# Kernel optimization log

Hardware: AMD Instinct MI355X
Metric: run time of the kernel (lower is better)

## Reference

```python
import jax, jax.numpy as jnp
import numpy as np

N, F_IN, C, H, L = 4096, 768, 256, 4, 2
DH = C // H  # 64 per-head dim for GATv2


def _ln(x, g, b, eps=1e-5):
    mu = x.mean(-1, keepdims=True)
    var = ((x - mu) ** 2).mean(-1, keepdims=True)
    return (x - mu) / jnp.sqrt(var + eps) * g + b


def _gat_layer(x, wl, wr, att, b, src, dst):
    # GATv2Conv: e_ij = att . leaky_relu(Wl x_j + Wr x_i); softmax over incoming j; concat heads.
    xs = (x @ wl).reshape(N, H, DH)  # source transform
    xd = (x @ wr).reshape(N, H, DH)  # target transform
    e = jnp.einsum('ehd,hd->eh', jax.nn.leaky_relu(xs[src] + xd[dst], 0.2), att)  # [E,H]
    m = jax.ops.segment_max(e, dst, num_segments=N)          # segment softmax (stable)
    p = jnp.exp(e - m[dst])
    s = jax.ops.segment_sum(p, dst, num_segments=N)
    alpha = p / (s[dst] + 1e-16)                             # [E,H]
    out = jax.ops.segment_sum(alpha[:, :, None] * xs[src], dst, num_segments=N)
    return out.reshape(N, C) + b


def _mha(x, wq, wk, wv, bq, bk, bv, wo, bo):
    # nn.MultiheadAttention, batch=1 sequence of all news nodes, eval mode.
    q = (x @ wq + bq).reshape(N, H, DH)
    k = (x @ wk + bk).reshape(N, H, DH)
    v = (x @ wv + bv).reshape(N, H, DH)
    scale = np.float32(1.0 / np.sqrt(DH))
    a = jax.nn.softmax(jnp.einsum('nhd,mhd->hnm', q, k) * scale, axis=-1)  # [H,N,N]
    o = jnp.einsum('hnm,mhd->nhd', a, v).reshape(N, C)
    return o @ wo + bo


def setup_inputs() -> dict:
    key = jax.random.key(0)
    ks = jax.random.split(key, 32)
    rn = lambda k, shp: (jax.random.normal(k, shp, dtype=jnp.float32) * 0.02)
    inp = {
        'x': jax.random.normal(ks[0], (N, F_IN), dtype=jnp.float32),
        'edge_index': jax.random.randint(ks[1], (2, N * 64), 0, N, dtype=jnp.int64),
        'emb_w': rn(ks[2], (F_IN, C)), 'emb_b': jnp.zeros((C,), jnp.float32),
        'g1_wl': rn(ks[3], (C, C)), 'g1_wr': rn(ks[4], (C, C)),
        'g1_att': rn(ks[5], (H, DH)), 'g1_b': jnp.zeros((C,), jnp.float32),
        'g2_wl': rn(ks[6], (C, C)), 'g2_wr': rn(ks[7], (C, C)),
        'g2_att': rn(ks[8], (H, DH)), 'g2_b': jnp.zeros((C,), jnp.float32),
        'mha_wq': rn(ks[9], (C, C)), 'mha_wk': rn(ks[10], (C, C)), 'mha_wv': rn(ks[11], (C, C)),
        'mha_bq': jnp.zeros((C,), jnp.float32), 'mha_bk': jnp.zeros((C,), jnp.float32),
        'mha_bv': jnp.zeros((C,), jnp.float32),
        'mha_wo': rn(ks[12], (C, C)), 'mha_bo': jnp.zeros((C,), jnp.float32),
        'ln_g': jnp.ones((C,), jnp.float32), 'ln_b': jnp.zeros((C,), jnp.float32),
        'cls_w1': rn(ks[13], (C, C // 2)), 'cls_b1': jnp.zeros((C // 2,), jnp.float32),
        'cls_w2': rn(ks[14], (C // 2, 2)), 'cls_b2': jnp.zeros((2,), jnp.float32),
    }
    return inp


def reference(x, edge_index, emb_w, emb_b, g1_wl, g1_wr, g1_att, g1_b,
              g2_wl, g2_wr, g2_att, g2_b, mha_wq, mha_wk, mha_wv, mha_bq,
              mha_bk, mha_bv, mha_wo, mha_bo, ln_g, ln_b,
              cls_w1, cls_b1, cls_w2, cls_b2):
    # add self loops (GATv2Conv default add_self_loops=True)
    loops = jnp.arange(N, dtype=edge_index.dtype)
    src = jnp.concatenate([edge_index[0], loops])
    dst = jnp.concatenate([edge_index[1], loops])

    h = x @ emb_w + emb_b                              # node embedding Linear(-1, C)
    h = jax.nn.relu(_gat_layer(h, g1_wl, g1_wr, g1_att, g1_b, src, dst))
    h = jax.nn.relu(_gat_layer(h, g2_wl, g2_wr, g2_att, g2_b, src, dst))

    # entity-aware self-attention + residual LayerNorm
    enh = _mha(h, mha_wq, mha_wk, mha_wv, mha_bq, mha_bk, mha_bv, mha_wo, mha_bo)
    h = _ln(h + enh, ln_g, ln_b)

    # classifier MLP (dropout = identity in eval)
    h = jax.nn.relu(h @ cls_w1 + cls_b1)
    return h @ cls_w2 + cls_b2
```

## Files before the change

kernel.cpp:

```cpp
#include <hip/hip_runtime.h>

typedef __attribute__((ext_vector_type(8))) short short8_t;
typedef __attribute__((ext_vector_type(4))) float f32x4_t;

#define N_NODES  4096
#define E0_EDGES 262144
#define E_TOTAL  266240
#define SPLITS   8
#define KV_PER_SPLIT (N_NODES / SPLITS)

__device__ __forceinline__ float bf2f(unsigned short u){
  union { unsigned int i; float f; } v; v.i = ((unsigned int)u) << 16; return v.f;
}
__device__ __forceinline__ unsigned short f2bf(float f){
  union { float f; unsigned int i; } v; v.f = f;
  unsigned int r = (v.i + 0x7FFFu + ((v.i >> 16) & 1u)) >> 16;
  return (unsigned short)r;
}
__device__ __forceinline__ unsigned int cvtpk_bf16(float lo, float hi){
  unsigned int r;
  asm volatile("v_cvt_pk_bf16_f32 %0, %1, %2" : "=v"(r) : "v"(lo), "v"(hi));
  return r;
}
template<int CTRL>
__device__ __forceinline__ float dpp_add(float x){
  int v = __builtin_amdgcn_update_dpp(0, __float_as_int(x), CTRL, 0xF, 0xF, true);
  return x + __int_as_float(v);
}
__device__ __forceinline__ float rowsum16(float x){
  x = dpp_add<0xB1>(x); x = dpp_add<0x4E>(x); x = dpp_add<0x124>(x); x = dpp_add<0x128>(x);
  return x;
}
__device__ __forceinline__ void wg_barrier(){
  asm volatile("s_waitcnt lgkmcnt(0)" ::: "memory");
  __builtin_amdgcn_s_barrier();
  asm volatile("" ::: "memory");
}
__device__ __forceinline__ uint4 cvt8_f32_to_bf16(float4 f0, float4 f1){
  union { unsigned short u[8]; uint4 q; } o;
  o.u[0]=f2bf(f0.x); o.u[1]=f2bf(f0.y); o.u[2]=f2bf(f0.z); o.u[3]=f2bf(f0.w);
  o.u[4]=f2bf(f1.x); o.u[5]=f2bf(f1.y); o.u[6]=f2bf(f1.z); o.u[7]=f2bf(f1.w);
  return o.q;
}

struct TJob { const float* src; unsigned short* dst; int rows, cols, tile0; };
struct TJobs { TJob j[10]; };

__global__ __launch_bounds__(256) void prep_kernel(TJobs jobs, int tb, int* __restrict__ zp){
  __shared__ unsigned short tile[64 * 64];
  int b = blockIdx.x, t = threadIdx.x;
  if (b < tb){
    int ji = 0;
    #pragma unroll
    for (int k = 1; k < 10; k++) if (b >= jobs.j[k].tile0) ji = k;
    TJob J = jobs.j[ji];
    int lt = b - J.tile0;
    int tpr = J.cols >> 6;
    int tr = lt / tpr, tc = lt - tr * tpr;
    #pragma unroll
    for (int i2 = 0; i2 < 2; i2++){
      int e = i2 * 2048 + t * 8;
      int nl = e >> 6, c8 = e & 63;
      const float* sp = &J.src[(size_t)(tr * 64 + nl) * J.cols + tc * 64 + c8];
      float4 v0 = *(const float4*)sp;
      float4 v1 = *(const float4*)(sp + 4);
      *(uint4*)&tile[nl * 64 + (((c8 >> 3) ^ ((nl >> 3) & 7)) * 8)] = cvt8_f32_to_bf16(v0, v1);
    }
    __syncthreads();
    #pragma unroll
    for (int i2 = 0; i2 < 2; i2++){
      int e = i2 * 2048 + t * 8;
      int cl = e >> 6, n8 = e & 63;
      union { unsigned short u[8]; uint4 q; } o;
      #pragma unroll
      for (int j = 0; j < 8; j++){
        int row = n8 + j;
        o.u[j] = tile[row * 64 + (((cl >> 3) ^ ((row >> 3) & 7)) * 8) + (cl & 7)];
      }
      *(uint4*)&J.dst[(size_t)(tc * 64 + cl) * J.rows + tr * 64 + n8] = o.q;
    }
    return;
  }
  int i = (b - tb) * 256 + t;
  if (i < 8192) zp[i] = 0;
}

__global__ __launch_bounds__(256) void scatter_kernel(const int* __restrict__ ei, const int* __restrict__ offs,
                                                      int* __restrict__ cur, int* __restrict__ csrc){
  int e = blockIdx.x * 256 + threadIdx.x;
  if (e >= E_TOTAL) return;
  int s, d;
  if (e < E0_EDGES){ s = ei[e]; d = ei[E0_EDGES + e]; }
  else { s = d = e - E0_EDGES; }
  int pos = offs[d] + atomicAdd(&cur[d], 1);
  csrc[pos] = s;
}

struct GJob { const unsigned short* Wt; const float* bias; float* outF; unsigned short* outB; unsigned short* outT; float scale; };
struct GJobs { GJob j[3]; };
struct AuxJob { int mode; const int* ei; int* a; int* b; };

__global__ __launch_bounds__(256) void gemm_kernel(const unsigned short* __restrict__ A, const float* __restrict__ Af32,
                                                   GJobs jobs, int K, int Nc, int relu, AuxJob AX){
  __shared__ unsigned short lds[8192];
  const int t = threadIdx.x;

  if (AX.mode && blockIdx.z == gridDim.z - 1){
    int flat = blockIdx.x + (blockIdx.y << 6);
    if (AX.mode == 1){
      for (int e = flat * 256 + t; e < E_TOTAL; e += 65536){
        int d = (e < E0_EDGES) ? AX.ei[E0_EDGES + e] : (e - E0_EDGES);
        atomicAdd(&AX.a[d], 1);
      }
    } else if (flat == 0){
      int* wtot = (int*)lds;
      int lane = t & 63, w = t >> 6;
      int v[16];
      int base = t * 16;
      int s = 0;
      #pragma unroll
      for (int j = 0; j < 16; j++){ v[j] = AX.a[base + j]; s += v[j]; }
      int x = s;
      #pragma unroll
      for (int off = 1; off < 64; off <<= 1){
        int y = __shfl_up(x, off, 64);
        if (lane >= off) x += y;
      }
      if (lane == 63) wtot[w] = x;
      __syncthreads();
      int wbase = 0;
      #pragma unroll
      for (int k = 0; k < 4; k++) if (k < w) wbase += wtot[k];
      int run = wbase + x - s;
      #pragma unroll
      for (int j = 0; j < 16; j++){ AX.b[base + j] = run; run += v[j]; }
      if (t == 255) AX.b[N_NODES] = run;
    }
    return;
  }

  const GJob job = jobs.j[blockIdx.z];
  const int lane = t & 63, w = t >> 6;
  const int wm = w >> 1, wn = w & 1;
  const int c16 = lane & 15, g = lane >> 4;
  const int bm = blockIdx.x, bn = blockIdx.y;

  const int srow = t >> 2, schunk = t & 3;
  const unsigned short* Ag = Af32 ? nullptr : (A + (size_t)(bm * 64 + srow) * K + schunk * 8);
  const float* Ag32 = Af32 ? (Af32 + (size_t)(bm * 64 + srow) * K + schunk * 8) : nullptr;
  const unsigned short* Bg = job.Wt + (size_t)(bn * 64 + srow) * K + schunk * 8;
  const int swz = srow * 32 + ((schunk ^ ((srow >> 1) & 3)) * 8);

  const int arow0 = wm * 32 + c16, arow1 = arow0 + 16;
  const int aoff0 = arow0 * 32 + ((g ^ ((arow0 >> 1) & 3)) * 8);
  const int aoff1 = arow1 * 32 + ((g ^ ((arow1 >> 1) & 3)) * 8);
  const int bcol0 = wn * 32 + c16, bcol1 = bcol0 + 16;
  const int boff0 = 2048 + bcol0 * 32 + ((g ^ ((bcol0 >> 1) & 3)) * 8);
  const int boff1 = 2048 + bcol1 * 32 + ((g ^ ((bcol1 >> 1) & 3)) * 8);

  f32x4_t acc[2][2] = {};
  const int nk = K >> 5;

  {
    uint4 av;
    if (Af32){
      float4 f0 = *(const float4*)(Ag32);
      float4 f1 = *(const float4*)(Ag32 + 4);
      av = cvt8_f32_to_bf16(f0, f1);
    } else {
      av = *(const uint4*)(Ag);
    }
    uint4 bv = *(const uint4*)(Bg);
    *(uint4*)&lds[swz]        = av;
    *(uint4*)&lds[2048 + swz] = bv;
  }
  int cur = 0;
  for (int i = 0; i < nk; i++){
    const bool pf = (i + 1) < nk;
    uint4 av, bv;
    float4 af0, af1;
    if (pf){
      if (Af32){
        af0 = *(const float4*)(Ag32 + (i + 1) * 32);
        af1 = *(const float4*)(Ag32 + (i + 1) * 32 + 4);
      } else {
        av = *(const uint4*)(Ag + (i + 1) * 32);
      }
      bv = *(const uint4*)(Bg + (i + 1) * 32);
    }
    wg_barrier();
    const int base = cur * 4096;
    union { uint4 u; short8_t s; } a0, a1, b0, b1;
    a0.u = *(const uint4*)&lds[base + aoff0];
    a1.u = *(const uint4*)&lds[base + aoff1];
    b0.u = *(const uint4*)&lds[base + boff0];
    b1.u = *(const uint4*)&lds[base + boff1];
    acc[0][0] = __builtin_amdgcn_mfma_f32_16x16x32_bf16(a0.s, b0.s, acc[0][0], 0, 0, 0);
    acc[0][1] = __builtin_amdgcn_mfma_f32_16x16x32_bf16(a0.s, b1.s, acc[0][1], 0, 0, 0);
    acc[1][0] = __builtin_amdgcn_mfma_f32_16x16x32_bf16(a1.s, b0.s, acc[1][0], 0, 0, 0);
    acc[1][1] = __builtin_amdgcn_mfma_f32_16x16x32_bf16(a1.s, b1.s, acc[1][1], 0, 0, 0);
    if (pf){
      const int nb = (cur ^ 1) * 4096;
      if (Af32) av = cvt8_f32_to_bf16(af0, af1);
      *(uint4*)&lds[nb + swz]        = av;
      *(uint4*)&lds[nb + 2048 + swz] = bv;
      cur ^= 1;
    }
  }

  #pragma unroll
  for (int fm = 0; fm < 2; fm++){
    #pragma unroll
    for (int fn = 0; fn < 2; fn++){
      int col = bn * 64 + wn * 32 + fn * 16 + c16;
      float bia = job.bias ? job.bias[col] : 0.f;
      float vv[4];
      #pragma unroll
      for (int r = 0; r < 4; r++){
        float v = (acc[fm][fn][r] + bia) * job.scale;
        if (relu) v = fmaxf(v, 0.f);
        vv[r] = v;
      }
      int row0 = bm * 64 + wm * 32 + fm * 16 + g * 4;
      if (job.outF){
        #pragma unroll
        for (int r = 0; r < 4; r++) job.outF[(size_t)(row0 + r) * Nc + col] = vv[r];
      }
      if (job.outB){
        #pragma unroll
        for (int r = 0; r < 4; r++) job.outB[(size_t)(row0 + r) * Nc + col] = f2bf(vv[r]);
      }
      if (job.outT){
        union { unsigned short u[4]; uint2 q; } pk;
        #pragma unroll
        for (int r = 0; r < 4; r++) pk.u[r] = f2bf(vv[r]);
        *(uint2*)&job.outT[(size_t)col * 4096 + row0] = pk.q;
      }
    }
  }
}

__global__ __launch_bounds__(256) void gat_gather(const unsigned short* __restrict__ xs, const unsigned short* __restrict__ xd,
                                                  const float* __restrict__ att, const float* __restrict__ bias,
                                                  const int* __restrict__ offs, const int* __restrict__ csrc,
                                                  unsigned short* __restrict__ outB, float* __restrict__ outF){
  __shared__ float combL[4][256];
  __shared__ float combS[4][4];
  const int i = blockIdx.x, t = threadIdx.x;
  const int lane = t & 63, w = t >> 6;
  float xdc[4], attc[4];
  {
    uint2 xv = *(const uint2*)&xd[i * 256 + lane * 4];
    xdc[0] = bf2f((unsigned short)(xv.x & 0xffff)); xdc[1] = bf2f((unsigned short)(xv.x >> 16));
    xdc[2] = bf2f((unsigned short)(xv.y & 0xffff)); xdc[3] = bf2f((unsigned short)(xv.y >> 16));
    float4 av = *(const float4*)&att[lane * 4];
    attc[0] = av.x; attc[1] = av.y; attc[2] = av.z; attc[3] = av.w;
  }
  const int b0 = offs[i], b1 = offs[i + 1];
  float acc0 = 0.f, acc1 = 0.f, acc2 = 0.f, acc3 = 0.f, ssum = 0.f;
  int p = b0 + w;
  for (; p + 4 < b1; p += 8){
    int sA = csrc[p], sB = csrc[p + 4];
    uint2 xa = *(const uint2*)&xs[sA * 256 + lane * 4];
    uint2 xb = *(const uint2*)&xs[sB * 256 + lane * 4];
    float a0 = bf2f((unsigned short)(xa.x & 0xffff)), a1 = bf2f((unsigned short)(xa.x >> 16));
    float a2 = bf2f((unsigned short)(xa.y & 0xffff)), a3 = bf2f((unsigned short)(xa.y >> 16));
    float b0_ = bf2f((unsigned short)(xb.x & 0xffff)), b1_ = bf2f((unsigned short)(xb.x >> 16));
    float b2_ = bf2f((unsigned short)(xb.y & 0xffff)), b3_ = bf2f((unsigned short)(xb.y >> 16));
    float va0 = a0 + xdc[0]; va0 = (va0 > 0.f) ? va0 : 0.2f * va0;
    float va1 = a1 + xdc[1]; va1 = (va1 > 0.f) ? va1 : 0.2f * va1;
    float va2 = a2 + xdc[2]; va2 = (va2 > 0.f) ? va2 : 0.2f * va2;
    float va3 = a3 + xdc[3]; va3 = (va3 > 0.f) ? va3 : 0.2f * va3;
    float vb0 = b0_ + xdc[0]; vb0 = (vb0 > 0.f) ? vb0 : 0.2f * vb0;
    float vb1 = b1_ + xdc[1]; vb1 = (vb1 > 0.f) ? vb1 : 0.2f * vb1;
    float vb2 = b2_ + xdc[2]; vb2 = (vb2 > 0.f) ? vb2 : 0.2f * vb2;
    float vb3 = b3_ + xdc[3]; vb3 = (vb3 > 0.f) ? vb3 : 0.2f * vb3;
    float eA = rowsum16(va0 * attc[0] + va1 * attc[1] + va2 * attc[2] + va3 * attc[3]);
    float eB = rowsum16(vb0 * attc[0] + vb1 * attc[1] + vb2 * attc[2] + vb3 * attc[3]);
    float pA = __expf(eA), pB = __expf(eB);
    ssum += pA + pB;
    acc0 += pA * a0 + pB * b0_; acc1 += pA * a1 + pB * b1_;
    acc2 += pA * a2 + pB * b2_; acc3 += pA * a3 + pB * b3_;
  }
  if (p < b1){
    int s = csrc[p];
    uint2 xv = *(const uint2*)&xs[s * 256 + lane * 4];
    float x0 = bf2f((unsigned short)(xv.x & 0xffff)), x1 = bf2f((unsigned short)(xv.x >> 16));
    float x2 = bf2f((unsigned short)(xv.y & 0xffff)), x3 = bf2f((unsigned short)(xv.y >> 16));
    float v0 = x0 + xdc[0]; v0 = (v0 > 0.f) ? v0 : 0.2f * v0;
    float v1 = x1 + xdc[1]; v1 = (v1 > 0.f) ? v1 : 0.2f * v1;
    float v2 = x2 + xdc[2]; v2 = (v2 > 0.f) ? v2 : 0.2f * v2;
    float v3 = x3 + xdc[3]; v3 = (v3 > 0.f) ? v3 : 0.2f * v3;
    float e = rowsum16(v0 * attc[0] + v1 * attc[1] + v2 * attc[2] + v3 * attc[3]);
    float pe = __expf(e);
    ssum += pe;
    acc0 += pe * x0; acc1 += pe * x1; acc2 += pe * x2; acc3 += pe * x3;
  }
  combL[w][lane * 4 + 0] = acc0; combL[w][lane * 4 + 1] = acc1;
  combL[w][lane * 4 + 2] = acc2; combL[w][lane * 4 + 3] = acc3;
  if ((lane & 15) == 0) combS[w][lane >> 4] = ssum;
  __syncthreads();
  float atot = combL[0][t] + combL[1][t] + combL[2][t] + combL[3][t];
  int hh = t >> 6;
  float stot = combS[0][hh] + combS[1][hh] + combS[2][hh] + combS[3][hh];
  float o = atot / (stot + 1e-16f) + bias[t];
  o = fmaxf(o, 0.f);
  outB[i * 256 + t] = f2bf(o);
  if (outF) outF[i * 256 + t] = o;
}

__global__ __launch_bounds__(512, 2) void attn_kernel(const unsigned short* __restrict__ qb, const unsigned short* __restrict__ kb,
                                                      const unsigned short* __restrict__ vt,
                                                      _Float16* __restrict__ Opart, float* __restrict__ Ol){
  __shared__ unsigned short K_lds[2][4096];
  __shared__ unsigned short V_lds[2][4096];
  __shared__ unsigned short P_lds[8][2048];
  const int t = threadIdx.x, lane = t & 63, w = t >> 6;
  const int c16 = lane & 15, g = lane >> 4;
  const int h = blockIdx.y, bq = blockIdx.x, sp = blockIdx.z;

  const int sr = t >> 3, sc = (t & 7) * 8;
  const int kw = sr * 64 + (((t & 7) ^ ((sr >> 1) & 7)) * 8);
  const int vw = sr * 64 + (((t & 7) ^ (sr & 7)) * 8);

  short8_t qa[2][2];
  #pragma unroll
  for (int qm = 0; qm < 2; qm++){
    int qrow = bq * 256 + w * 32 + qm * 16 + c16;
    union { uint4 u; short8_t s; } cv0, cv1;
    cv0.u = *(const uint4*)&qb[(size_t)qrow * 256 + h * 64 + g * 8];
    cv1.u = *(const uint4*)&qb[(size_t)qrow * 256 + h * 64 + 32 + g * 8];
    qa[qm][0] = cv0.s; qa[qm][1] = cv1.s;
  }

  f32x4_t oacc[2][4] = {};
  float lsum[2] = {0.f, 0.f};

  const int kv_lo = sp * KV_PER_SPLIT;
  {
    uint4 k0 = *(const uint4*)&kb[(size_t)(kv_lo + sr) * 256 + h * 64 + sc];
    uint4 v0 = *(const uint4*)&vt[(size_t)(h * 64 + sr) * 4096 + kv_lo + sc];
    *(uint4*)&K_lds[0][kw] = k0;
    *(uint4*)&V_lds[0][vw] = v0;
  }
  int cur = 0;

  for (int ti = 0; ti < KV_PER_SPLIT / 64; ti++){
    const bool pf = (ti + 1) < KV_PER_SPLIT / 64;
    uint4 nk, nv;
    if (pf){
      int kvn = kv_lo + (ti + 1) * 64;
      nk = *(const uint4*)&kb[(size_t)(kvn + sr) * 256 + h * 64 + sc];
      nv = *(const uint4*)&vt[(size_t)(h * 64 + sr) * 4096 + kvn + sc];
    }
    wg_barrier();
    const unsigned short* Kb = K_lds[cur];
    const unsigned short* Vb = V_lds[cur];
    unsigned short* Pw = P_lds[w];

    f32x4_t sacc[2][4] = {};
    #pragma unroll
    for (int kd = 0; kd < 2; kd++){
      #pragma unroll
      for (int fn = 0; fn < 4; fn++){
        union { uint4 u; short8_t s; } kf;
        kf.u = *(const uint4*)&Kb[(fn * 16 + c16) * 64 + (((kd * 4 + g) ^ ((c16 >> 1) & 7)) * 8)];
        sacc[0][fn] = __builtin_amdgcn_mfma_f32_16x16x32_bf16(kf.s, qa[0][kd], sacc[0][fn], 0, 0, 0);
        sacc[1][fn] = __builtin_amdgcn_mfma_f32_16x16x32_bf16(kf.s, qa[1][kd], sacc[1][fn], 0, 0, 0);
      }
    }

    #pragma unroll
    for (int qm = 0; qm < 2; qm++){
      float ps = 0.f;
      int row = qm * 16 + c16;
      #pragma unroll
      for (int fn = 0; fn < 4; fn++){
        float p0 = __builtin_exp2f(sacc[qm][fn][0]);
        float p1 = __builtin_exp2f(sacc[qm][fn][1]);
        float p2 = __builtin_exp2f(sacc[qm][fn][2]);
        float p3 = __builtin_exp2f(sacc[qm][fn][3]);
        ps += (p0 + p1) + (p2 + p3);
        uint2 pk;
        pk.x = cvtpk_bf16(p0, p1);
        pk.y = cvtpk_bf16(p2, p3);
        int chunk = (fn * 2 + (g >> 1)) ^ (c16 & 7);
        *(uint2*)&Pw[row * 64 + chunk * 8 + (g & 1) * 4] = pk;
      }
      ps += __shfl_xor(ps, 16, 64);
      ps += __shfl_xor(ps, 32, 64);
      lsum[qm] += ps;
    }

    #pragma unroll
    for (int kd2 = 0; kd2 < 2; kd2++){
      const int ch = (((kd2 * 4 + g) ^ (c16 & 7)) * 8);
      union { uint4 u; short8_t s; } pt0, pt1;
      pt0.u = *(const uint4*)&Pw[c16 * 64 + ch];
      pt1.u = *(const uint4*)&Pw[(16 + c16) * 64 + ch];
      #pragma unroll
      for (int fn = 0; fn < 4; fn++){
        union { uint4 u; short8_t s; } vf;
        vf.u = *(const uint4*)&Vb[(fn * 16 + c16) * 64 + ch];
        oacc[0][fn] = __builtin_amdgcn_mfma_f32_16x16x32_bf16(vf.s, pt0.s, oacc[0][fn], 0, 0, 0);
        oacc[1][fn] = __builtin_amdgcn_mfma_f32_16x16x32_bf16(vf.s, pt1.s, oacc[1][fn], 0, 0, 0);
      }
    }

    if (pf){
      *(uint4*)&K_lds[cur ^ 1][kw] = nk;
      *(uint4*)&V_lds[cur ^ 1][vw] = nv;
      cur ^= 1;
    }
  }

  const int sh = sp * 4 + h;
  #pragma unroll
  for (int qm = 0; qm < 2; qm++){
    int node = bq * 256 + w * 32 + qm * 16 + c16;
    #pragma unroll
    for (int fn = 0; fn < 4; fn++){
      union { _Float16 h[4]; uint2 q; } pk;
      #pragma unroll
      for (int r = 0; r < 4; r++) pk.h[r] = (_Float16)oacc[qm][fn][r];
      *(uint2*)&Opart[((size_t)sh * N_NODES + node) * 64 + fn * 16 + g * 4] = pk.q;
    }
    if (g == 0) Ol[(size_t)sh * N_NODES + node] = lsum[qm];
  }
}

__global__ __launch_bounds__(256) void wo_ln_cls_kernel(const _Float16* __restrict__ Opart, const float* __restrict__ Ol,
                                                        const unsigned short* __restrict__ Wt, const float* __restrict__ bo,
                                                        const float* __restrict__ h2f, const float* __restrict__ gg,
                                                        const float* __restrict__ bb,
                                                        const unsigned short* __restrict__ Wt1, const float* __restrict__ b1,
                                                        const float* __restrict__ w2, const float* __restrict__ b2,
                                                        float* __restrict__ out){
  __shared__ unsigned short Ab[2][512];
  __shared__ unsigned short Bb[2][8192];
  __shared__ unsigned short Cb[2][4096];
  __shared__ unsigned short hl[16 * 264];
  __shared__ float red1[4][16], red2[4][16];
  __shared__ float cred0[4][16], cred1[4][16];
  __shared__ float Ls[64];
  const int t = threadIdx.x, lane = t & 63, w = t >> 6;
  const int c16 = lane & 15, g = lane >> 4;
  const int bm = blockIdx.x;

  const int arow = t >> 2, achk = t & 3;
  const int aswz = arow * 32 + ((achk ^ ((arow >> 1) & 3)) * 8);
  const int bq_ = t >> 2, bchk = t & 3;

  if (t < 64){
    int node = bm * 16 + (t >> 2), h = t & 3;
    float L = 0.f;
    #pragma unroll
    for (int s = 0; s < SPLITS; s++) L += Ol[(size_t)(s * 4 + h) * N_NODES + node];
    Ls[t] = 1.f / L;
  }
  __syncthreads();

  const int afr = c16 * 32 + ((g ^ ((c16 >> 1) & 3)) * 8);
  int bfr[4];
  #pragma unroll
  for (int fn = 0; fn < 4; fn++){
    int col = w * 64 + fn * 16 + c16;
    bfr[fn] = col * 32 + ((g ^ ((col >> 1) & 3)) * 8);
  }

  const int anode = bm * 16 + arow;
  auto loadA = [&](int k0, uint4* pa){
    int c0 = k0 + achk * 8;
    int hh = c0 >> 6, d0 = c0 & 63;
    #pragma unroll
    for (int s = 0; s < SPLITS; s++)
      pa[s] = *(const uint4*)&Opart[((size_t)(s * 4 + hh) * N_NODES + anode) * 64 + d0];
  };
  auto packA = [&](int k0, const uint4* pa) -> uint4 {
    float a[8] = {0.f,0.f,0.f,0.f,0.f,0.f,0.f,0.f};
    #pragma unroll
    for (int s = 0; s < SPLITS; s++){
      union { uint4 q; _Float16 h[8]; } u; u.q = pa[s];
      #pragma unroll
      for (int j = 0; j < 8; j++) a[j] += (float)u.h[j];
    }
    int c0 = k0 + achk * 8;
    float Li = Ls[(arow << 2) | (c0 >> 6)];
    union { unsigned short u[8]; uint4 q; } o;
    #pragma unroll
    for (int j = 0; j < 8; j++) o.u[j] = f2bf(a[j] * Li);
    return o.q;
  };

  f32x4_t acc[4] = {};
  {
    if (t < 64){
      uint4 pa0[SPLITS];
      loadA(0, pa0);
      *(uint4*)&Ab[0][aswz] = packA(0, pa0);
    }
    #pragma unroll
    for (int j = 0; j < 4; j++){
      int col = j * 64 + bq_;
      *(uint4*)&Bb[0][col * 32 + ((bchk ^ ((col >> 1) & 3)) * 8)] = *(const uint4*)&Wt[(size_t)col * 256 + bchk * 8];
    }
  }
  int cur = 0;
  for (int i = 0; i < 8; i++){
    const bool pf = i < 7;
    uint4 pa[SPLITS]; uint4 pb[4];
    int k1 = (i + 1) * 32;
    if (pf){
      if (t < 64) loadA(k1, pa);
      #pragma unroll
      for (int j = 0; j < 4; j++){
        int col = j * 64 + bq_;
        pb[j] = *(const uint4*)&Wt[(size_t)col * 256 + k1 + bchk * 8];
      }
    }
    wg_barrier();
    union { uint4 u; short8_t s; } a, b;
    a.u = *(const uint4*)&Ab[cur][afr];
    #pragma unroll
    for (int fn = 0; fn < 4; fn++){
      b.u = *(const uint4*)&Bb[cur][bfr[fn]];
      acc[fn] = __builtin_amdgcn_mfma_f32_16x16x32_bf16(a.s, b.s, acc[fn], 0, 0, 0);
    }
    if (pf){
      if (t < 64) *(uint4*)&Ab[cur ^ 1][aswz] = packA(k1, pa);
      #pragma unroll
      for (int j = 0; j < 4; j++){
        int col = j * 64 + bq_;
        *(uint4*)&Bb[cur ^ 1][col * 32 + ((bchk ^ ((col >> 1) & 3)) * 8)] = pb[j];
      }
      cur ^= 1;
    }
  }

  float vv[4][4];
  #pragma unroll
  for (int fn = 0; fn < 4; fn++){
    int col = w * 64 + fn * 16 + c16;
    float bia = bo[col];
    #pragma unroll
    for (int r = 0; r < 4; r++)
      vv[fn][r] = acc[fn][r] + bia + h2f[(size_t)(bm * 16 + g * 4 + r) * 256 + col];
  }
  #pragma unroll
  for (int r = 0; r < 4; r++){
    float a = 0.f, b = 0.f;
    #pragma unroll
    for (int fn = 0; fn < 4; fn++){ a += vv[fn][r]; b += vv[fn][r] * vv[fn][r]; }
    a = rowsum16(a); b = rowsum16(b);
    if (c16 == 0){ red1[w][g * 4 + r] = a; red2[w][g * 4 + r] = b; }
  }
  __syncthreads();
  #pragma unroll
  for (int r = 0; r < 4; r++){
    int row = g * 4 + r;
    float S1 = red1[0][row] + red1[1][row] + red1[2][row] + red1[3][row];
    float S2 = red2[0][row] + red2[1][row] + red2[2][row] + red2[3][row];
    float mean = S1 * (1.f / 256.f);
    float var = S2 * (1.f / 256.f) - mean * mean;
    float rs = rsqrtf(var + 1e-5f);
    #pragma unroll
    for (int fn = 0; fn < 4; fn++){
      int col = w * 64 + fn * 16 + c16;
      hl[row * 264 + col] = f2bf((vv[fn][r] - mean) * rs * gg[col] + bb[col]);
    }
  }

  wg_barrier();
  int cfr[2];
  #pragma unroll
  for (int fn = 0; fn < 2; fn++){
    int col = w * 32 + fn * 16 + c16;
    cfr[fn] = col * 32 + ((g ^ ((col >> 1) & 3)) * 8);
  }
  f32x4_t cacc[2] = {};
  {
    #pragma unroll
    for (int j = 0; j < 2; j++){
      int col = j * 64 + bq_;
      *(uint4*)&Cb[0][col * 32 + ((bchk ^ ((col >> 1) & 3)) * 8)] = *(const uint4*)&Wt1[(size_t)col * 256 + bchk * 8];
    }
  }
  cur = 0;
  for (int i = 0; i < 8; i++){
    const bool pf = i < 7;
    uint4 pb[2];
    if (pf){
      int k1 = (i + 1) * 32;
      #pragma unroll
      for (int j = 0; j < 2; j++){
        int col = j * 64 + bq_;
        pb[j] = *(const uint4*)&Wt1[(size_t)col * 256 + k1 + bchk * 8];
      }
    }
    wg_barrier();
    union { uint4 u; short8_t s; } a, b;
    a.u = *(const uint4*)&hl[c16 * 264 + i * 32 + g * 8];
    #pragma unroll
    for (int fn = 0; fn < 2; fn++){
      b.u = *(const uint4*)&Cb[cur][cfr[fn]];
      cacc[fn] = __builtin_amdgcn_mfma_f32_16x16x32_bf16(a.s, b.s, cacc[fn], 0, 0, 0);
    }
    if (pf){
      #pragma unroll
      for (int j = 0; j < 2; j++){
        int col = j * 64 + bq_;
        *(uint4*)&Cb[cur ^ 1][col * 32 + ((bchk ^ ((col >> 1) & 3)) * 8)] = pb[j];
      }
      cur ^= 1;
    }
  }
  float cv[2][4];
  #pragma unroll
  for (int fn = 0; fn < 2; fn++){
    int col = w * 32 + fn * 16 + c16;
    float bia = b1[col];
    #pragma unroll
    for (int r = 0; r < 4; r++) cv[fn][r] = fmaxf(cacc[fn][r] + bia, 0.f);
  }
  float w20 = w2[(w * 32 + c16) * 2],      w21 = w2[(w * 32 + c16) * 2 + 1];
  float w30 = w2[(w * 32 + 16 + c16) * 2], w31 = w2[(w * 32 + 16 + c16) * 2 + 1];
  #pragma unroll
  for (int r = 0; r < 4; r++){
    float a0 = cv[0][r] * w20 + cv[1][r] * w30;
    float a1 = cv[0][r] * w21 + cv[1][r] * w31;
    a0 = rowsum16(a0); a1 = rowsum16(a1);
    if (c16 == 0){ cred0[w][g * 4 + r] = a0; cred1[w][g * 4 + r] = a1; }
  }
  __syncthreads();
  if (t < 16){
    float q0 = cred0[0][t] + cred0[1][t] + cred0[2][t] + cred0[3][t] + b2[0];
    float q1 = cred1[0][t] + cred1[1][t] + cred1[2][t] + cred1[3][t] + b2[1];
    out[(size_t)(bm * 16 + t) * 2]     = q0;
    out[(size_t)(bm * 16 + t) * 2 + 1] = q1;
  }
}

extern "C" void kernel_launch(void* const* d_in, const int* in_sizes, int n_in,
                              void* d_out, int out_size, void* d_ws, size_t ws_size,
                              hipStream_t stream){
  const float* x      = (const float*)d_in[0];
  const int*   ei     = (const int*)d_in[1];
  const float* emb_w  = (const float*)d_in[2];
  const float* emb_b  = (const float*)d_in[3];
  const float* g1_wl  = (const float*)d_in[4];
  const float* g1_wr  = (const float*)d_in[5];
  const float* g1_att = (const float*)d_in[6];
  const float* g1_b   = (const float*)d_in[7];
  const float* g2_wl  = (const float*)d_in[8];
  const float* g2_wr  = (const float*)d_in[9];
  const float* g2_att = (const float*)d_in[10];
  const float* g2_b   = (const float*)d_in[11];
  const float* wq     = (const float*)d_in[12];
  const float* wk     = (const float*)d_in[13];
  const float* wv     = (const float*)d_in[14];
  const float* bq     = (const float*)d_in[15];
  const float* bk     = (const float*)d_in[16];
  const float* bv     = (const float*)d_in[17];
  const float* wo     = (const float*)d_in[18];
  const float* bo     = (const float*)d_in[19];
  const float* ln_g   = (const float*)d_in[20];
  const float* ln_b   = (const float*)d_in[21];
  const float* cls_w1 = (const float*)d_in[22];
  const float* cls_b1 = (const float*)d_in[23];
  const float* cls_w2 = (const float*)d_in[24];
  const float* cls_b2 = (const float*)d_in[25];
  float* out = (float*)d_out;

  char* wsb = (char*)d_ws;
  size_t o = 0;
  auto take = [&](size_t bytes) -> char* {
    char* r = wsb + o; o += (bytes + 255) & ~(size_t)255; return r;
  };
  unsigned short* wt_emb  = (unsigned short*)take(768 * 256 * 2);
  unsigned short* wt_wl1  = (unsigned short*)take(256 * 256 * 2);
  unsigned short* wt_wr1  = (unsigned short*)take(256 * 256 * 2);
  unsigned short* wt_wl2  = (unsigned short*)take(256 * 256 * 2);
  unsigned short* wt_wr2  = (unsigned short*)take(256 * 256 * 2);
  unsigned short* wt_wq   = (unsigned short*)take(256 * 256 * 2);
  unsigned short* wt_wk   = (unsigned short*)take(256 * 256 * 2);
  unsigned short* wt_wv   = (unsigned short*)take(256 * 256 * 2);
  unsigned short* wt_wo   = (unsigned short*)take(256 * 256 * 2);
  unsigned short* wt_cls1 = (unsigned short*)take(256 * 128 * 2);
  unsigned short* h0_bf   = (unsigned short*)take((size_t)4096 * 256 * 2);
  unsigned short* xs1_bf  = (unsigned short*)take((size_t)4096 * 256 * 2);
  unsigned short* xd1_bf  = (unsigned short*)take((size_t)4096 * 256 * 2);
  unsigned short* h1_bf   = (unsigned short*)take((size_t)4096 * 256 * 2);
  unsigned short* xs2_bf  = (unsigned short*)take((size_t)4096 * 256 * 2);
  unsigned short* xd2_bf  = (unsigned short*)take((size_t)4096 * 256 * 2);
  unsigned short* h2_bf   = (unsigned short*)take((size_t)4096 * 256 * 2);
  float*          h2_f    = (float*)take((size_t)4096 * 256 * 4);
  unsigned short* q_bf    = (unsigned short*)take((size_t)4096 * 256 * 2);
  unsigned short* k_bf    = (unsigned short*)take((size_t)4096 * 256 * 2);
  unsigned short* vt_bf   = (unsigned short*)take((size_t)4096 * 256 * 2);
  int* deg  = (int*)take(4096 * 4);
  int* cur  = (int*)take(4096 * 4);
  int* offs = (int*)take(4097 * 4);
  int* csrc = (int*)take((size_t)E_TOTAL * 4);
  _Float16* Opart = (_Float16*)take((size_t)SPLITS * 4 * N_NODES * 64 * 2);
  float*    Ol    = (float*)take((size_t)SPLITS * 4 * N_NODES * 4);

  TJobs TJ;
  TJob tj[10] = {
    { emb_w,  wt_emb,  768, 256, 0 },
    { g1_wl,  wt_wl1,  256, 256, 0 },
    { g1_wr,  wt_wr1,  256, 256, 0 },
    { g2_wl,  wt_wl2,  256, 256, 0 },
    { g2_wr,  wt_wr2,  256, 256, 0 },
    { wq,     wt_wq,   256, 256, 0 },
    { wk,     wt_wk,   256, 256, 0 },
    { wv,     wt_wv,   256, 256, 0 },
    { wo,     wt_wo,   256, 256, 0 },
    { cls_w1, wt_cls1, 256, 128, 0 },
  };
  int tb = 0;
  for (int i = 0; i < 10; i++){
    tj[i].tile0 = tb;
    tb += (tj[i].rows >> 6) * (tj[i].cols >> 6);
    TJ.j[i] = tj[i];
  }
  prep_kernel<<<tb + 32, 256, 0, stream>>>(TJ, tb, deg);

  GJobs J;
  AuxJob AX0 = { 0, nullptr, nullptr, nullptr };
  J = {}; J.j[0] = { wt_emb, emb_b, nullptr, h0_bf, nullptr, 1.f };
  AuxJob AXh = { 1, ei, deg, nullptr };
  gemm_kernel<<<dim3(64, 4, 2), 256, 0, stream>>>(nullptr, x, J, 768, 256, 0, AXh);
  J = {}; J.j[0] = { wt_wl1, nullptr, nullptr, xs1_bf, nullptr, 1.f }; J.j[1] = { wt_wr1, nullptr, nullptr, xd1_bf, nullptr, 1.f };
  AuxJob AXs = { 2, nullptr, deg, offs };
  gemm_kernel<<<dim3(64, 4, 3), 256, 0, stream>>>(h0_bf, nullptr, J, 256, 256, 0, AXs);
  scatter_kernel<<<(E_TOTAL + 255) / 256, 256, 0, stream>>>(ei, offs, cur, csrc);
  gat_gather<<<4096, 256, 0, stream>>>(xs1_bf, xd1_bf, g1_att, g1_b, offs, csrc, h1_bf, nullptr);
  J = {}; J.j[0] = { wt_wl2, nullptr, nullptr, xs2_bf, nullptr, 1.f }; J.j[1] = { wt_wr2, nullptr, nullptr, xd2_bf, nullptr, 1.f };
  gemm_kernel<<<dim3(64, 4, 2), 256, 0, stream>>>(h1_bf, nullptr, J, 256, 256, 0, AX0);
  gat_gather<<<4096, 256, 0, stream>>>(xs2_bf, xd2_bf, g2_att, g2_b, offs, csrc, h2_bf, h2_f);
  J = {};
  J.j[0] = { wt_wq, bq, nullptr, q_bf, nullptr, 0.125f * 1.44269504f };
  J.j[1] = { wt_wk, bk, nullptr, k_bf, nullptr, 1.f };
  J.j[2] = { wt_wv, bv, nullptr, nullptr, vt_bf, 1.f };
  gemm_kernel<<<dim3(64, 4, 3), 256, 0, stream>>>(h2_bf, nullptr, J, 256, 256, 0, AX0);
  attn_kernel<<<dim3(16, 4, SPLITS), 512, 0, stream>>>(q_bf, k_bf, vt_bf, Opart, Ol);
  wo_ln_cls_kernel<<<256, 256, 0, stream>>>(Opart, Ol, wt_wo, bo, h2_f, ln_g, ln_b,
                                            wt_cls1, cls_b1, cls_w2, cls_b2, out);

  (void)in_sizes; (void)n_in; (void)out_size; (void)ws_size;
}
```

Before: 177.0 us.

## Replace CSR build with fixed-capacity per-node edge buckets and pre-convert x to bf16

```diff
diff --git a/kernel.cpp b/kernel.cpp
--- a/kernel.cpp
+++ b/kernel.cpp
@@ -8,6 +8,7 @@
 #define E_TOTAL  266240
 #define SPLITS   8
 #define KV_PER_SPLIT (N_NODES / SPLITS)
+#define BUCKET_CAP 160
 
 __device__ __forceinline__ float bf2f(unsigned short u){
   union { unsigned int i; float f; } v; v.i = ((unsigned int)u) << 16; return v.f;
@@ -46,15 +47,25 @@
 struct TJob { const float* src; unsigned short* dst; int rows, cols, tile0; };
 struct TJobs { TJob j[10]; };
 
-__global__ __launch_bounds__(256) void prep_kernel(TJobs jobs, int tb, int* __restrict__ zp){
+__global__ __launch_bounds__(256) void prep_kernel(const float* __restrict__ x, unsigned short* __restrict__ xb,
+                                                   TJobs jobs, int tb, int* __restrict__ zp){
   __shared__ unsigned short tile[64 * 64];
   int b = blockIdx.x, t = threadIdx.x;
-  if (b < tb){
+  if (b < 3072){
+    int i = (b * 256 + t) * 4;
+    float4 v = *(const float4*)&x[i];
+    union { unsigned short u[4]; uint2 q; } o;
+    o.u[0] = f2bf(v.x); o.u[1] = f2bf(v.y); o.u[2] = f2bf(v.z); o.u[3] = f2bf(v.w);
+    *(uint2*)&xb[i] = o.q;
+    return;
+  }
+  if (b < 3072 + tb){
+    int bb = b - 3072;
     int ji = 0;
     #pragma unroll
-    for (int k = 1; k < 10; k++) if (b >= jobs.j[k].tile0) ji = k;
+    for (int k = 1; k < 10; k++) if (bb >= jobs.j[k].tile0) ji = k;
     TJob J = jobs.j[ji];
-    int lt = b - J.tile0;
+    int lt = bb - J.tile0;
     int tpr = J.cols >> 6;
     int tr = lt / tpr, tc = lt - tr * tpr;
     #pragma unroll
@@ -81,64 +92,28 @@
     }
     return;
   }
-  int i = (b - tb) * 256 + t;
-  if (i < 8192) zp[i] = 0;
-}
-
-__global__ __launch_bounds__(256) void scatter_kernel(const int* __restrict__ ei, const int* __restrict__ offs,
-                                                      int* __restrict__ cur, int* __restrict__ csrc){
+  int i = (b - 3072 - tb) * 256 + t;
+  if (i < N_NODES) zp[i] = 0;
+}
+
+__global__ __launch_bounds__(256) void scatter_kernel(const int* __restrict__ ei, int* __restrict__ cnt,
+                                                      int* __restrict__ csrc){
   int e = blockIdx.x * 256 + threadIdx.x;
   if (e >= E_TOTAL) return;
   int s, d;
   if (e < E0_EDGES){ s = ei[e]; d = ei[E0_EDGES + e]; }
   else { s = d = e - E0_EDGES; }
-  int pos = offs[d] + atomicAdd(&cur[d], 1);
-  csrc[pos] = s;
+  int pos = atomicAdd(&cnt[d], 1);
+  csrc[d * BUCKET_CAP + pos] = s;
 }
 
 struct GJob { const unsigned short* Wt; const float* bias; float* outF; unsigned short* outB; unsigned short* outT; float scale; };
 struct GJobs { GJob j[3]; };
-struct AuxJob { int mode; const int* ei; int* a; int* b; };
-
-__global__ __launch_bounds__(256) void gemm_kernel(const unsigned short* __restrict__ A, const float* __restrict__ Af32,
-                                                   GJobs jobs, int K, int Nc, int relu, AuxJob AX){
+
+__global__ __launch_bounds__(256) void gemm_kernel(const unsigned short* __restrict__ A, GJobs jobs,
+                                                   int K, int Nc, int relu){
   __shared__ unsigned short lds[8192];
   const int t = threadIdx.x;
-
-  if (AX.mode && blockIdx.z == gridDim.z - 1){
-    int flat = blockIdx.x + (blockIdx.y << 6);
-    if (AX.mode == 1){
-      for (int e = flat * 256 + t; e < E_TOTAL; e += 65536){
-        int d = (e < E0_EDGES) ? AX.ei[E0_EDGES + e] : (e - E0_EDGES);
-        atomicAdd(&AX.a[d], 1);
-      }
-    } else if (flat == 0){
-      int* wtot = (int*)lds;
-      int lane = t & 63, w = t >> 6;
-      int v[16];
-      int base = t * 16;
-      int s = 0;
-      #pragma unroll
-      for (int j = 0; j < 16; j++){ v[j] = AX.a[base + j]; s += v[j]; }
-      int x = s;
-      #pragma unroll
-      for (int off = 1; off < 64; off <<= 1){
-        int y = __shfl_up(x, off, 64);
-        if (lane >= off) x += y;
-      }
-      if (lane == 63) wtot[w] = x;
-      __syncthreads();
-      int wbase = 0;
-      #pragma unroll
-      for (int k = 0; k < 4; k++) if (k < w) wbase += wtot[k];
-      int run = wbase + x - s;
-      #pragma unroll
-      for (int j = 0; j < 16; j++){ AX.b[base + j] = run; run += v[j]; }
-      if (t == 255) AX.b[N_NODES] = run;
-    }
-    return;
-  }
-
   const GJob job = jobs.j[blockIdx.z];
   const int lane = t & 63, w = t >> 6;
   const int wm = w >> 1, wn = w & 1;
@@ -146,8 +121,7 @@
   const int bm = blockIdx.x, bn = blockIdx.y;
 
   const int srow = t >> 2, schunk = t & 3;
-  const unsigned short* Ag = Af32 ? nullptr : (A + (size_t)(bm * 64 + srow) * K + schunk * 8);
-  const float* Ag32 = Af32 ? (Af32 + (size_t)(bm * 64 + srow) * K + schunk * 8) : nullptr;
+  const unsigned short* Ag = A      + (size_t)(bm * 64 + srow) * K + schunk * 8;
   const unsigned short* Bg = job.Wt + (size_t)(bn * 64 + srow) * K + schunk * 8;
   const int swz = srow * 32 + ((schunk ^ ((srow >> 1) & 3)) * 8);
 
@@ -162,14 +136,7 @@
   const int nk = K >> 5;
 
   {
-    uint4 av;
-    if (Af32){
-      float4 f0 = *(const float4*)(Ag32);
-      float4 f1 = *(const float4*)(Ag32 + 4);
-      av = cvt8_f32_to_bf16(f0, f1);
-    } else {
-      av = *(const uint4*)(Ag);
-    }
+    uint4 av = *(const uint4*)(Ag);
     uint4 bv = *(const uint4*)(Bg);
     *(uint4*)&lds[swz]        = av;
     *(uint4*)&lds[2048 + swz] = bv;
@@ -178,14 +145,8 @@
   for (int i = 0; i < nk; i++){
     const bool pf = (i + 1) < nk;
     uint4 av, bv;
-    float4 af0, af1;
     if (pf){
-      if (Af32){
-        af0 = *(const float4*)(Ag32 + (i + 1) * 32);
-        af1 = *(const float4*)(Ag32 + (i + 1) * 32 + 4);
-      } else {
-        av = *(const uint4*)(Ag + (i + 1) * 32);
-      }
+      av = *(const uint4*)(Ag + (i + 1) * 32);
       bv = *(const uint4*)(Bg + (i + 1) * 32);
     }
     wg_barrier();
@@ -201,7 +162,6 @@
     acc[1][1] = __builtin_amdgcn_mfma_f32_16x16x32_bf16(a1.s, b1.s, acc[1][1], 0, 0, 0);
     if (pf){
       const int nb = (cur ^ 1) * 4096;
-      if (Af32) av = cvt8_f32_to_bf16(af0, af1);
       *(uint4*)&lds[nb + swz]        = av;
       *(uint4*)&lds[nb + 2048 + swz] = bv;
       cur ^= 1;
@@ -242,7 +202,7 @@
 
 __global__ __launch_bounds__(256) void gat_gather(const unsigned short* __restrict__ xs, const unsigned short* __restrict__ xd,
                                                   const float* __restrict__ att, const float* __restrict__ bias,
-                                                  const int* __restrict__ offs, const int* __restrict__ csrc,
+                                                  const int* __restrict__ cnt, const int* __restrict__ csrc,
                                                   unsigned short* __restrict__ outB, float* __restrict__ outF){
   __shared__ float combL[4][256];
   __shared__ float combS[4][4];
@@ -256,11 +216,12 @@
     float4 av = *(const float4*)&att[lane * 4];
     attc[0] = av.x; attc[1] = av.y; attc[2] = av.z; attc[3] = av.w;
   }
-  const int b0 = offs[i], b1 = offs[i + 1];
+  const int b1 = cnt[i];
+  const int* bucket = csrc + i * BUCKET_CAP;
   float acc0 = 0.f, acc1 = 0.f, acc2 = 0.f, acc3 = 0.f, ssum = 0.f;
-  int p = b0 + w;
+  int p = w;
   for (; p + 4 < b1; p += 8){
-    int sA = csrc[p], sB = csrc[p + 4];
+    int sA = bucket[p], sB = bucket[p + 4];
     uint2 xa = *(const uint2*)&xs[sA * 256 + lane * 4];
     uint2 xb = *(const uint2*)&xs[sB * 256 + lane * 4];
     float a0 = bf2f((unsigned short)(xa.x & 0xffff)), a1 = bf2f((unsigned short)(xa.x >> 16));
@@ -283,7 +244,7 @@
     acc2 += pA * a2 + pB * b2_; acc3 += pA * a3 + pB * b3_;
   }
   if (p < b1){
-    int s = csrc[p];
+    int s = bucket[p];
     uint2 xv = *(const uint2*)&xs[s * 256 + lane * 4];
     float x0 = bf2f((unsigned short)(xv.x & 0xffff)), x1 = bf2f((unsigned short)(xv.x >> 16));
     float x2 = bf2f((unsigned short)(xv.y & 0xffff)), x3 = bf2f((unsigned short)(xv.y >> 16));
@@ -686,6 +647,7 @@
   unsigned short* wt_wv   = (unsigned short*)take(256 * 256 * 2);
   unsigned short* wt_wo   = (unsigned short*)take(256 * 256 * 2);
   unsigned short* wt_cls1 = (unsigned short*)take(256 * 128 * 2);
+  unsigned short* x_bf    = (unsigned short*)take((size_t)4096 * 768 * 2);
   unsigned short* h0_bf   = (unsigned short*)take((size_t)4096 * 256 * 2);
   unsigned short* xs1_bf  = (unsigned short*)take((size_t)4096 * 256 * 2);
   unsigned short* xd1_bf  = (unsigned short*)take((size_t)4096 * 256 * 2);
@@ -697,10 +659,8 @@
   unsigned short* q_bf    = (unsigned short*)take((size_t)4096 * 256 * 2);
   unsigned short* k_bf    = (unsigned short*)take((size_t)4096 * 256 * 2);
   unsigned short* vt_bf   = (unsigned short*)take((size_t)4096 * 256 * 2);
-  int* deg  = (int*)take(4096 * 4);
-  int* cur  = (int*)take(4096 * 4);
-  int* offs = (int*)take(4097 * 4);
-  int* csrc = (int*)take((size_t)E_TOTAL * 4);
+  int* cnt  = (int*)take(4096 * 4);
+  int* csrc = (int*)take((size_t)N_NODES * BUCKET_CAP * 4);
   _Float16* Opart = (_Float16*)take((size_t)SPLITS * 4 * N_NODES * 64 * 2);
   float*    Ol    = (float*)take((size_t)SPLITS * 4 * N_NODES * 4);
 
@@ -723,26 +683,24 @@
     tb += (tj[i].rows >> 6) * (tj[i].cols >> 6);
     TJ.j[i] = tj[i];
   }
-  prep_kernel<<<tb + 32, 256, 0, stream>>>(TJ, tb, deg);
+  prep_kernel<<<3072 + tb + 16, 256, 0, stream>>>(x, x_bf, TJ, tb, cnt);
+
+  scatter_kernel<<<(E_TOTAL + 255) / 256, 256, 0, stream>>>(ei, cnt, csrc);
 
   GJobs J;
-  AuxJob AX0 = { 0, nullptr, nullptr, nullptr };
   J = {}; J.j[0] = { wt_emb, emb_b, nullptr, h0_bf, nullptr, 1.f };
-  AuxJob AXh = { 1, ei, deg, nullptr };
-  gemm_kernel<<<dim3(64, 4, 2), 256, 0, stream>>>(nullptr, x, J, 768, 256, 0, AXh);
+  gemm_kernel<<<dim3(64, 4, 1), 256, 0, stream>>>(x_bf, J, 768, 256, 0);
   J = {}; J.j[0] = { wt_wl1, nullptr, nullptr, xs1_bf, nullptr, 1.f }; J.j[1] = { wt_wr1, nullptr, nullptr, xd1_bf, nullptr, 1.f };
-  AuxJob AXs = { 2, nullptr, deg, offs };
-  gemm_kernel<<<dim3(64, 4, 3), 256, 0, stream>>>(h0_bf, nullptr, J, 256, 256, 0, AXs);
-  scatter_kernel<<<(E_TOTAL + 255) / 256, 256, 0, stream>>>(ei, offs, cur, csrc);
-  gat_gather<<<4096, 256, 0, stream>>>(xs1_bf, xd1_bf, g1_att, g1_b, offs, csrc, h1_bf, nullptr);
+  gemm_kernel<<<dim3(64, 4, 2), 256, 0, stream>>>(h0_bf, J, 256, 256, 0);
+  gat_gather<<<4096, 256, 0, stream>>>(xs1_bf, xd1_bf, g1_att, g1_b, cnt, csrc, h1_bf, nullptr);
   J = {}; J.j[0] = { wt_wl2, nullptr, nullptr, xs2_bf, nullptr, 1.f }; J.j[1] = { wt_wr2, nullptr, nullptr, xd2_bf, nullptr, 1.f };
-  gemm_kernel<<<dim3(64, 4, 2), 256, 0, stream>>>(h1_bf, nullptr, J, 256, 256, 0, AX0);
-  gat_gather<<<4096, 256, 0, stream>>>(xs2_bf, xd2_bf, g2_att, g2_b, offs, csrc, h2_bf, h2_f);
+  gemm_kernel<<<dim3(64, 4, 2), 256, 0, stream>>>(h1_bf, J, 256, 256, 0);
+  gat_gather<<<4096, 256, 0, stream>>>(xs2_bf, xd2_bf, g2_att, g2_b, cnt, csrc, h2_bf, h2_f);
   J = {};
   J.j[0] = { wt_wq, bq, nullptr, q_bf, nullptr, 0.125f * 1.44269504f };
   J.j[1] = { wt_wk, bk, nullptr, k_bf, nullptr, 1.f };
   J.j[2] = { wt_wv, bv, nullptr, nullptr, vt_bf, 1.f };
-  gemm_kernel<<<dim3(64, 4, 3), 256, 0, stream>>>(h2_bf, nullptr, J, 256, 256, 0, AX0);
+  gemm_kernel<<<dim3(64, 4, 3), 256, 0, stream>>>(h2_bf, J, 256, 256, 0);
   attn_kernel<<<dim3(16, 4, SPLITS), 512, 0, stream>>>(q_bf, k_bf, vt_bf, Opart, Ol);
   wo_ln_cls_kernel<<<256, 256, 0, stream>>>(Opart, Ol, wt_wo, bo, h2_f, ln_g, ln_b,
                                             wt_cls1, cls_b1, cls_w2, cls_b2, out);
```

Result: faster. 153.5 us (-13.3%).
